# Kernel tuning notes

Measured on AMD Instinct MI355X. Metric: run time of the kernel, lower is better.

The kernel has to match this reference:

```python
import jax, jax.numpy as jnp
import numpy as np

B, N, M, D0, D, H, KW = 2, 512, 512, 1024, 100, 50, 7
K_SLOPE, X0_SIG = 20.0, 0.5  # LogisticActivation(x0=0.5, k=20), k not trained


def setup_inputs() -> dict:
    key = jax.random.key(0)
    ks = jax.random.split(key, 8)
    s = lambda k, shp: jax.random.normal(k, shp, jnp.float32) * 0.05
    return {
        "x0": jax.random.normal(ks[0], (B, N, D0), jnp.float32),
        "x1": jax.random.normal(ks[1], (B, M, D0), jnp.float32),
        "W_proj": s(ks[2], (D0, D)),
        "b_proj": jnp.zeros((D,), jnp.float32),
        "W_hid": s(ks[3], (2 * D, H)),
        "b_hid": jnp.zeros((H,), jnp.float32),
        "conv_w": s(ks[4], (1, H, KW, KW)),  # OIHW
        "conv_b": jnp.zeros((1,), jnp.float32),
        "theta": jnp.array([0.5], jnp.float32),
        "lambda_": jnp.array([0.3], jnp.float32),
        "gamma": jnp.array([0.2], jnp.float32),
    }


def reference(x0, x1, W_proj, b_proj, W_hid, b_hid, conv_w, conv_b, theta, lambda_, gamma):
    # --- embedding: FullyConnectedEmbed (Linear + ReLU) ---
    e0 = jax.nn.relu(x0 @ W_proj + b_proj)  # [B,N,D]
    e1 = jax.nn.relu(x1 @ W_proj + b_proj)  # [B,M,D]
    # --- contact: broadcast features -> 1x1 conv -> 7x7 conv -> sigmoid ---
    diff = jnp.abs(e0[:, :, None, :] - e1[:, None, :, :])   # [B,N,M,D]
    mul = e0[:, :, None, :] * e1[:, None, :, :]             # [B,N,M,D]
    Z = jnp.concatenate([diff, mul], axis=-1)               # [B,N,M,2D]
    Hh = jax.nn.relu(jnp.einsum('bnmc,ch->bhnm', Z, W_hid) + b_hid[None, :, None, None])
    C = jax.lax.conv_general_dilated(Hh, conv_w, (1, 1), 'SAME')
    C = jax.nn.sigmoid(C + conv_b[None, :, None, None])     # [B,1,N,M]
    # --- weighting matrix W (do_w=True) ---
    i = jnp.arange(N, dtype=jnp.float32)
    j = jnp.arange(M, dtype=jnp.float32)
    a = -jnp.square((i + 1 - (N + 1) / 2) / (-(N + 1) / 2))
    b = -jnp.square((j + 1 - (M + 1) / 2) / (-(M + 1) / 2))
    a = jnp.exp(lambda_ * a)                                 # [N]
    b = jnp.exp(lambda_ * b)                                 # [M]
    W = (1 - theta[0]) * (a[:, None] * b[None, :]) + theta[0]
    yhat = C * W                                             # [B,1,N,M]
    # --- global pooling: mean/var threshold + ratio ---
    mu = jnp.mean(yhat, axis=(1, 2, 3), keepdims=True)
    sigma = jnp.var(yhat, axis=(1, 2, 3), ddof=1, keepdims=True)  # torch.var is unbiased
    Q = jax.nn.relu(yhat - mu - gamma[0] * sigma)
    phat = jnp.sum(Q, axis=(1, 2, 3)) / (jnp.sum(jnp.sign(Q), axis=(1, 2, 3)) + 1)
    # --- LogisticActivation ---
    return jnp.clip(1.0 / (1.0 + jnp.exp(-K_SLOPE * (phat - X0_SIG))), 0.0, 1.0)  # [B]
```

## Files before the change

### kernel.cpp

```cpp
#include <hip/hip_runtime.h>
#include <hip/hip_bf16.h>

static constexpr int Bc   = 2;
static constexpr int Nc   = 512;
static constexpr int Mc   = 512;
static constexpr int D0c  = 1024;
static constexpr int Dc   = 100;
static constexpr int Hc   = 50;
static constexpr long long NMc = (long long)Nc * Mc;

typedef __attribute__((ext_vector_type(8))) short short8v;
typedef __attribute__((ext_vector_type(4))) float f32x4;

__device__ __forceinline__ unsigned pk_hi(float a, float b) {
  return __builtin_amdgcn_perm(__float_as_uint(b), __float_as_uint(a), 0x07060302u);
}
__device__ __forceinline__ float trunc16(float x) {
  return __uint_as_float(__float_as_uint(x) & 0xffff0000u);
}

__global__ __launch_bounds__(512) void k_embed(
    const float* __restrict__ x0, const float* __restrict__ x1,
    const float* __restrict__ Wp, const float* __restrict__ bp,
    float* __restrict__ e0, float* __restrict__ e1)
{
  __shared__ float xs[8][1024];
  const int t   = threadIdx.x;
  const int rg0 = blockIdx.x * 8;

  #pragma unroll
  for (int i = 0; i < 4; ++i) {
    const int idx = i*512 + t;
    const int r   = idx >> 8;
    const int c4  = idx & 255;
    const int rgs = rg0 + r;
    const float* src = (rgs < Bc*Nc) ? (x0 + (size_t)rgs * D0c)
                                     : (x1 + (size_t)(rgs - Bc*Nc) * D0c);
    *(float4*)&xs[r][c4*4] = *(const float4*)&src[c4*4];
  }
  __syncthreads();

  const int c = t & 127;
  const int q = t >> 7;
  if (c < Dc) {
    const int row0 = q*2, row1 = q*2 + 1;
    float acc0 = 0.f, acc1 = 0.f;
    for (int k = 0; k < D0c; k += 8) {
      float w[8];
      #pragma unroll
      for (int u = 0; u < 8; ++u) w[u] = Wp[(k+u)*Dc + c];
      const float4 xa0 = *(const float4*)&xs[row0][k];
      const float4 xb0 = *(const float4*)&xs[row0][k+4];
      const float4 xa1 = *(const float4*)&xs[row1][k];
      const float4 xb1 = *(const float4*)&xs[row1][k+4];
      acc0 = fmaf(xa0.x, w[0], acc0); acc1 = fmaf(xa1.x, w[0], acc1);
      acc0 = fmaf(xa0.y, w[1], acc0); acc1 = fmaf(xa1.y, w[1], acc1);
      acc0 = fmaf(xa0.z, w[2], acc0); acc1 = fmaf(xa1.z, w[2], acc1);
      acc0 = fmaf(xa0.w, w[3], acc0); acc1 = fmaf(xa1.w, w[3], acc1);
      acc0 = fmaf(xb0.x, w[4], acc0); acc1 = fmaf(xb1.x, w[4], acc1);
      acc0 = fmaf(xb0.y, w[5], acc0); acc1 = fmaf(xb1.y, w[5], acc1);
      acc0 = fmaf(xb0.z, w[6], acc0); acc1 = fmaf(xb1.z, w[6], acc1);
      acc0 = fmaf(xb0.w, w[7], acc0); acc1 = fmaf(xb1.w, w[7], acc1);
    }
    const float bias = bp[c];
    {
      const int rg = rg0 + row0;
      const float v = fmaxf(acc0 + bias, 0.f);
      if (rg < Bc*Nc) e0[(size_t)rg*Dc + c] = v;
      else            e1[(size_t)(rg - Bc*Nc)*Dc + c] = v;
    }
    {
      const int rg = rg0 + row1;
      const float v = fmaxf(acc1 + bias, 0.f);
      if (rg < Bc*Nc) e0[(size_t)rg*Dc + c] = v;
      else            e1[(size_t)(rg - Bc*Nc)*Dc + c] = v;
    }
  }
}

__global__ __launch_bounds__(64) void k_wsplit(
    const float* __restrict__ Whid, uint4* __restrict__ wsplit)
{
  const int fi = blockIdx.x;
  const int s  = fi >> 3;
  const int ht = (fi >> 1) & 3;
  const int hl = fi & 1;
  const int lane = threadIdx.x;
  const int h_loc = lane & 15, g = lane >> 4;
  const int h = ht*16 + h_loc;
  uint dw[4] = {0u,0u,0u,0u};
  #pragma unroll
  for (int j = 0; j < 8; ++j) {
    const int p = j >> 2, q = j & 3;
    const int d = s*16 + g*4 + q;
    float wv = (h < Hc && d < Dc) ? Whid[(size_t)(p*Dc + d)*Hc + h] : 0.f;
    const uint bits = __float_as_uint(wv);
    const uint hi_bits = bits & 0xffff0000u;
    uint e16;
    if (hl == 0) e16 = hi_bits >> 16;
    else {
      const float lo = wv - __uint_as_float(hi_bits);
      e16 = __float_as_uint(lo) >> 16;
    }
    dw[j >> 1] |= e16 << (16 * (j & 1));
  }
  uint4 v; v.x = dw[0]; v.y = dw[1]; v.z = dw[2]; v.w = dw[3];
  wsplit[fi*64 + lane] = v;
}

__global__ __launch_bounds__(256, 4) void k_hh(
    const float* __restrict__ e0, const float* __restrict__ e1,
    const uint4* __restrict__ wsplit, const float* __restrict__ bhid,
    float* __restrict__ hh, int slab_n0, int slabh)
{
  const int b   = blockIdx.z;
  const int lr0 = blockIdx.y * 2;
  const int n0base = slab_n0 + lr0;
  if (n0base + 1 < 0 || n0base >= Nc) return;

  __shared__ float e1T[32][116];
  __shared__ float e0s[2][112];
  __shared__ float biasl[64];
  __shared__ float ldsT[4][16][17];

  const int t   = threadIdx.x;
  const int m0b = blockIdx.x * 32;

  {
    const int row = t >> 3;
    const int cb  = (t & 7) * 4;
    const float* src = e1 + (size_t)(b*Mc + m0b + row) * Dc;
    #pragma unroll
    for (int pass = 0; pass < 4; ++pass) {
      const int col = cb + pass*32;
      if (col < 112) {
        float4 v = {0.f,0.f,0.f,0.f};
        if (col < Dc) v = *(const float4*)&src[col];
        *(float4*)&e1T[row][col] = v;
      }
    }
  }
  {
    const int nl2 = t >> 7, col = t & 127;
    if (col < 112) {
      const int n = n0base + nl2;
      float v = 0.f;
      if ((unsigned)n < (unsigned)Nc && col < Dc)
        v = e0[(size_t)(b*Nc + n)*Dc + col];
      e0s[nl2][col] = v;
    }
  }
  if (t < 64) biasl[t] = (t < Hc) ? bhid[t] : 0.f;
  __syncthreads();

  const int w = t >> 6, lane = t & 63;
  const int cl = lane & 15, g = lane >> 4;
  const int nl   = w >> 1;
  const int mrow = (w & 1) * 16 + cl;

  f32x4 acc0 = {0.f,0.f,0.f,0.f}, acc1 = {0.f,0.f,0.f,0.f};
  f32x4 acc2 = {0.f,0.f,0.f,0.f}, acc3 = {0.f,0.f,0.f,0.f};

  union U { uint4 u; short8v v; };
  const uint4* __restrict__ wq = wsplit + lane;

  #pragma unroll
  for (int s = 0; s < 7; ++s) {
    const int d0 = s*16 + g*4;
    const float4 E1 = *(const float4*)&e1T[mrow][d0];
    const float4 E0 = *(const float4*)&e0s[nl][d0];

    const float df0 = fabsf(E0.x - E1.x), df1 = fabsf(E0.y - E1.y),
                df2 = fabsf(E0.z - E1.z), df3 = fabsf(E0.w - E1.w);
    const float pm0 = E0.x*E1.x, pm1 = E0.y*E1.y,
                pm2 = E0.z*E1.z, pm3 = E0.w*E1.w;

    U ahi, alo;
    ahi.u.x = pk_hi(df0, df1); ahi.u.y = pk_hi(df2, df3);
    ahi.u.z = pk_hi(pm0, pm1); ahi.u.w = pk_hi(pm2, pm3);
    alo.u.x = pk_hi(df0 - trunc16(df0), df1 - trunc16(df1));
    alo.u.y = pk_hi(df2 - trunc16(df2), df3 - trunc16(df3));
    alo.u.z = pk_hi(pm0 - trunc16(pm0), pm1 - trunc16(pm1));
    alo.u.w = pk_hi(pm2 - trunc16(pm2), pm3 - trunc16(pm3));

    #pragma unroll
    for (int ht = 0; ht < 4; ++ht) {
      U whi, wlo;
      whi.u = wq[((s*4 + ht)*2 + 0)*64];
      wlo.u = wq[((s*4 + ht)*2 + 1)*64];
      f32x4* ac = (ht == 0) ? &acc0 : (ht == 1) ? &acc1 : (ht == 2) ? &acc2 : &acc3;
      *ac = __builtin_amdgcn_mfma_f32_16x16x32_bf16(ahi.v, whi.v, *ac, 0, 0, 0);
      *ac = __builtin_amdgcn_mfma_f32_16x16x32_bf16(alo.v, whi.v, *ac, 0, 0, 0);
      *ac = __builtin_amdgcn_mfma_f32_16x16x32_bf16(ahi.v, wlo.v, *ac, 0, 0, 0);
    }
  }

  const int n = n0base + nl;
  const bool nvalid = (unsigned)n < (unsigned)Nc;
  const int S = slabh * Mc;
  float* hhp = hh + ((size_t)b*Hc)*S + (size_t)(lr0 + nl)*Mc
                  + (m0b + (w & 1)*16 + cl) + (size_t)g*S;

  const f32x4 accs[4] = {acc0, acc1, acc2, acc3};
  #pragma unroll
  for (int ht = 0; ht < 4; ++ht) {
    #pragma unroll
    for (int r = 0; r < 4; ++r) ldsT[w][cl][g*4 + r] = accs[ht][r];
    #pragma unroll
    for (int p = 0; p < 4; ++p) {
      const int hl2 = p*4 + g;
      const int h = ht*16 + hl2;
      if (h < Hc && nvalid) {
        const float v = fmaxf(ldsT[w][hl2][cl] + biasl[h], 0.f);
        hhp[(size_t)((ht*16 + p*4) * S)] = v;
      }
    }
  }
}

__global__ __launch_bounds__(256) void k_conv(
    const float* __restrict__ hh, const float* __restrict__ cw,
    const float* __restrict__ cb, const float* __restrict__ theta,
    const float* __restrict__ lam, float* __restrict__ yhat,
    double* __restrict__ gacc, int n_begin, int slabh)
{
  __shared__ float tile[2][38*40];
  __shared__ double red[2][4];
  const int t  = threadIdx.x;
  const int b  = blockIdx.z;
  const int n0 = n_begin + blockIdx.y * 32;
  const int m0 = blockIdx.x * 32;

  const int rr = t >> 3;
  const int c0 = 4 * (t & 7);

  float stg[6];
  auto issue = [&](int h) {
    #pragma unroll
    for (int it = 0; it < 6; ++it) {
      const int idx = it*256 + t;
      float v = 0.f;
      if (idx < 38*38) {
        const int r = idx / 38, c = idx - r*38;
        const int gn = n0 - 3 + r, gm = m0 - 3 + c;
        if ((unsigned)gn < (unsigned)Nc && (unsigned)gm < (unsigned)Mc)
          v = hh[(((size_t)(b*Hc + h))*slabh + (gn - n_begin + 3))*Mc + gm];
      }
      stg[it] = v;
    }
  };
  auto commit = [&](int buf) {
    #pragma unroll
    for (int it = 0; it < 6; ++it) {
      const int idx = it*256 + t;
      if (idx < 38*38) {
        const int r = idx / 38, c = idx - r*38;
        tile[buf][r*40 + c] = stg[it];
      }
    }
  };

  issue(0); commit(0);
  __syncthreads();

  float acc0 = 0.f, acc1 = 0.f, acc2 = 0.f, acc3 = 0.f;
  for (int h = 0; h < Hc; ++h) {
    if (h + 1 < Hc) issue(h + 1);
    const int buf = h & 1;
    const float* __restrict__ cp = cw + h*49;
    #pragma unroll
    for (int dn = 0; dn < 7; ++dn) {
      const float* tp = &tile[buf][(rr+dn)*40 + c0];
      const float4 wa = *(const float4*)tp;
      const float4 wb = *(const float4*)(tp+4);
      const float2 wc = *(const float2*)(tp+8);
      const float w_[10] = {wa.x,wa.y,wa.z,wa.w, wb.x,wb.y,wb.z,wb.w, wc.x,wc.y};
      #pragma unroll
      for (int dm = 0; dm < 7; ++dm) {
        const float wv = cp[dn*7 + dm];
        acc0 = fmaf(w_[dm],   wv, acc0);
        acc1 = fmaf(w_[dm+1], wv, acc1);
        acc2 = fmaf(w_[dm+2], wv, acc2);
        acc3 = fmaf(w_[dm+3], wv, acc3);
      }
    }
    if (h + 1 < Hc) { commit((h+1) & 1); __syncthreads(); }
  }

  const float th  = theta[0];
  const float lm  = lam[0];
  const float cbv = cb[0];
  const int n = n0 + rr;
  const int m = m0 + c0;
  const float half1 = 0.5f * (float)(Nc + 1);
  const float inv   = 1.0f / half1;
  const float ti  = ((float)(n+1) - half1) * inv;
  const float av  = expf(-lm * ti * ti);
  float y[4];
  double s = 0.0, ss = 0.0;
  const float a_[4] = {acc0, acc1, acc2, acc3};
  #pragma unroll
  for (int j = 0; j < 4; ++j) {
    const float tj = ((float)(m+1+j) - half1) * inv;
    const float bv = expf(-lm * tj * tj);
    const float sg = 1.f / (1.f + expf(-(a_[j] + cbv)));
    y[j] = sg * ((1.f - th) * av * bv + th);
    s  += (double)y[j];
    ss += (double)y[j] * (double)y[j];
  }
  float4 yv; yv.x = y[0]; yv.y = y[1]; yv.z = y[2]; yv.w = y[3];
  *(float4*)&yhat[((size_t)(b*Nc + n))*Mc + m] = yv;

  for (int off = 32; off > 0; off >>= 1) {
    s  += __shfl_down(s,  off);
    ss += __shfl_down(ss, off);
  }
  const int wave = t >> 6, lane = t & 63;
  if (lane == 0) { red[0][wave] = s; red[1][wave] = ss; }
  __syncthreads();
  if (t == 0) {
    atomicAdd(&gacc[b*4 + 0], red[0][0] + red[0][1] + red[0][2] + red[0][3]);
    atomicAdd(&gacc[b*4 + 1], red[1][0] + red[1][1] + red[1][2] + red[1][3]);
  }
}

__global__ __launch_bounds__(256) void k_q(
    const float* __restrict__ yhat, double* __restrict__ gacc,
    const float* __restrict__ gamma)
{
  const int tid = blockIdx.x * 256 + threadIdx.x;
  const int b = blockIdx.x >> 8;
  const float4 y = ((const float4*)yhat)[tid];
  const double sum = gacc[b*4 + 0], ssq = gacc[b*4 + 1];
  const double mu  = sum / (double)NMc;
  const double var = (ssq - sum * mu) / ((double)NMc - 1.0);
  const double thr = mu + (double)gamma[0] * var;

  double sq = 0.0; int c = 0;
  double q;
  q = (double)y.x - thr; if (q > 0.0) { sq += q; ++c; }
  q = (double)y.y - thr; if (q > 0.0) { sq += q; ++c; }
  q = (double)y.z - thr; if (q > 0.0) { sq += q; ++c; }
  q = (double)y.w - thr; if (q > 0.0) { sq += q; ++c; }

  for (int off = 32; off > 0; off >>= 1) {
    sq += __shfl_down(sq, off);
    c  += __shfl_down(c,  off);
  }
  __shared__ double sr[4];
  __shared__ int    cr[4];
  const int wave = threadIdx.x >> 6, lane = threadIdx.x & 63;
  if (lane == 0) { sr[wave] = sq; cr[wave] = c; }
  __syncthreads();
  if (threadIdx.x == 0) {
    atomicAdd(&gacc[b*4 + 2], sr[0] + sr[1] + sr[2] + sr[3]);
    atomicAdd(&gacc[b*4 + 3], (double)(cr[0] + cr[1] + cr[2] + cr[3]));
  }
}

__global__ void k_out(const double* __restrict__ gacc, float* __restrict__ out)
{
  const int t = threadIdx.x;
  if (t < Bc) {
    const double phat = gacc[t*4 + 2] / (gacc[t*4 + 3] + 1.0);
    double v = 1.0 / (1.0 + exp(-20.0 * (phat - 0.5)));
    v = fmin(fmax(v, 0.0), 1.0);
    out[t] = (float)v;
  }
}

extern "C" void kernel_launch(void* const* d_in, const int* in_sizes, int n_in,
                              void* d_out, int out_size, void* d_ws, size_t ws_size,
                              hipStream_t stream)
{
  const float* x0 = (const float*)d_in[0];
  const float* x1 = (const float*)d_in[1];
  const float* Wp = (const float*)d_in[2];
  const float* bp = (const float*)d_in[3];
  const float* Wh = (const float*)d_in[4];
  const float* bh = (const float*)d_in[5];
  const float* cw = (const float*)d_in[6];
  const float* cb = (const float*)d_in[7];
  const float* th = (const float*)d_in[8];
  const float* lm = (const float*)d_in[9];
  const float* gm = (const float*)d_in[10];
  float* out = (float*)d_out;
  (void)in_sizes; (void)n_in; (void)out_size;

  int slabrows, nslab;
  if      (ws_size >= (size_t)109232128) { slabrows = 512; nslab = 1; }
  else if (ws_size >= (size_t)56803328)  { slabrows = 256; nslab = 2; }
  else                                    { slabrows = 128; nslab = 4; }
  const int slabh = slabrows + 6;
  const size_t hh_bytes = (size_t)slabh * 204800;

  char* ws = (char*)d_ws;
  float*  e0   = (float*)(ws);
  float*  e1   = (float*)(ws + 409600);
  double* gacc = (double*)(ws + 819200);
  uint4*  wsp  = (uint4*)(ws + 884736);
  float*  hh   = (float*)(ws + 1048576);
  float*  yhat = (float*)(ws + 1048576 + hh_bytes);

  hipMemsetAsync(gacc, 0, 64, stream);
  k_wsplit<<<dim3(56), dim3(64), 0, stream>>>(Wh, wsp);
  k_embed<<<dim3(256), dim3(512), 0, stream>>>(x0, x1, Wp, bp, e0, e1);
  for (int s = 0; s < nslab; ++s) {
    const int n_begin = s * slabrows;
    k_hh  <<<dim3(16, slabh/2, 2), dim3(256), 0, stream>>>(
        e0, e1, wsp, bh, hh, n_begin - 3, slabh);
    k_conv<<<dim3(16, slabrows / 32, 2), dim3(256), 0, stream>>>(
        hh, cw, cb, th, lm, yhat, gacc, n_begin, slabh);
  }
  k_q  <<<dim3(512), dim3(256), 0, stream>>>(yhat, gacc, gm);
  k_out<<<dim3(1),   dim3(64),  0, stream>>>(gacc, out);
}
```

Baseline: 283.7 us.

## Store hidden maps as bf16, split conv over channel halves, fuse small kernels

Result: slower. 382.0 us (+34.6%).

```diff
diff --git a/kernel.cpp b/kernel.cpp
--- a/kernel.cpp
+++ b/kernel.cpp
@@ -18,14 +18,52 @@
 __device__ __forceinline__ float trunc16(float x) {
   return __uint_as_float(__float_as_uint(x) & 0xffff0000u);
 }
-
-__global__ __launch_bounds__(512) void k_embed(
+__device__ __forceinline__ unsigned short f2bf_rne(float x) {
+  const unsigned b = __float_as_uint(x);
+  const unsigned r = b + 0x7fffu + ((b >> 16) & 1u);
+  return (unsigned short)(r >> 16);
+}
+
+__global__ __launch_bounds__(512) void k_prep(
     const float* __restrict__ x0, const float* __restrict__ x1,
     const float* __restrict__ Wp, const float* __restrict__ bp,
-    float* __restrict__ e0, float* __restrict__ e1)
-{
+    const float* __restrict__ Whid,
+    float* __restrict__ e0, float* __restrict__ e1,
+    uint4* __restrict__ wsplit, double* __restrict__ gacc)
+{
+  const int t = threadIdx.x;
+  if (blockIdx.x == 256) {
+    if (t < 18) ((int*)gacc)[t] = 0;
+    const int grp = t >> 6, lane = t & 63;
+    const int h_loc = lane & 15, g = lane >> 4;
+    for (int fi = grp; fi < 56; fi += 8) {
+      const int s  = fi >> 3;
+      const int ht = (fi >> 1) & 3;
+      const int hl = fi & 1;
+      const int h = ht*16 + h_loc;
+      uint dw[4] = {0u,0u,0u,0u};
+      #pragma unroll
+      for (int j = 0; j < 8; ++j) {
+        const int p = j >> 2, q = j & 3;
+        const int d = s*16 + g*4 + q;
+        float wv = (h < Hc && d < Dc) ? Whid[(size_t)(p*Dc + d)*Hc + h] : 0.f;
+        const uint bits = __float_as_uint(wv);
+        const uint hi_bits = bits & 0xffff0000u;
+        uint e16;
+        if (hl == 0) e16 = hi_bits >> 16;
+        else {
+          const float lo = wv - __uint_as_float(hi_bits);
+          e16 = __float_as_uint(lo) >> 16;
+        }
+        dw[j >> 1] |= e16 << (16 * (j & 1));
+      }
+      uint4 v; v.x = dw[0]; v.y = dw[1]; v.z = dw[2]; v.w = dw[3];
+      wsplit[fi*64 + lane] = v;
+    }
+    return;
+  }
+
   __shared__ float xs[8][1024];
-  const int t   = threadIdx.x;
   const int rg0 = blockIdx.x * 8;
 
   #pragma unroll
@@ -78,40 +116,10 @@
   }
 }
 
-__global__ __launch_bounds__(64) void k_wsplit(
-    const float* __restrict__ Whid, uint4* __restrict__ wsplit)
-{
-  const int fi = blockIdx.x;
-  const int s  = fi >> 3;
-  const int ht = (fi >> 1) & 3;
-  const int hl = fi & 1;
-  const int lane = threadIdx.x;
-  const int h_loc = lane & 15, g = lane >> 4;
-  const int h = ht*16 + h_loc;
-  uint dw[4] = {0u,0u,0u,0u};
-  #pragma unroll
-  for (int j = 0; j < 8; ++j) {
-    const int p = j >> 2, q = j & 3;
-    const int d = s*16 + g*4 + q;
-    float wv = (h < Hc && d < Dc) ? Whid[(size_t)(p*Dc + d)*Hc + h] : 0.f;
-    const uint bits = __float_as_uint(wv);
-    const uint hi_bits = bits & 0xffff0000u;
-    uint e16;
-    if (hl == 0) e16 = hi_bits >> 16;
-    else {
-      const float lo = wv - __uint_as_float(hi_bits);
-      e16 = __float_as_uint(lo) >> 16;
-    }
-    dw[j >> 1] |= e16 << (16 * (j & 1));
-  }
-  uint4 v; v.x = dw[0]; v.y = dw[1]; v.z = dw[2]; v.w = dw[3];
-  wsplit[fi*64 + lane] = v;
-}
-
 __global__ __launch_bounds__(256, 4) void k_hh(
     const float* __restrict__ e0, const float* __restrict__ e1,
     const uint4* __restrict__ wsplit, const float* __restrict__ bhid,
-    float* __restrict__ hh, int slab_n0, int slabh)
+    unsigned short* __restrict__ hh, int slab_n0, int slabh)
 {
   const int b   = blockIdx.z;
   const int lr0 = blockIdx.y * 2;
@@ -198,7 +206,7 @@
   const int n = n0base + nl;
   const bool nvalid = (unsigned)n < (unsigned)Nc;
   const int S = slabh * Mc;
-  float* hhp = hh + ((size_t)b*Hc)*S + (size_t)(lr0 + nl)*Mc
+  unsigned short* hhp = hh + ((size_t)b*Hc)*S + (size_t)(lr0 + nl)*Mc
                   + (m0b + (w & 1)*16 + cl) + (size_t)g*S;
 
   const f32x4 accs[4] = {acc0, acc1, acc2, acc3};
@@ -212,22 +220,21 @@
       const int h = ht*16 + hl2;
       if (h < Hc && nvalid) {
         const float v = fmaxf(ldsT[w][hl2][cl] + biasl[h], 0.f);
-        hhp[(size_t)((ht*16 + p*4) * S)] = v;
+        hhp[(size_t)((ht*16 + p*4) * S)] = f2bf_rne(v);
       }
     }
   }
 }
 
 __global__ __launch_bounds__(256) void k_conv(
-    const float* __restrict__ hh, const float* __restrict__ cw,
-    const float* __restrict__ cb, const float* __restrict__ theta,
-    const float* __restrict__ lam, float* __restrict__ yhat,
-    double* __restrict__ gacc, int n_begin, int slabh)
+    const unsigned short* __restrict__ hh, const float* __restrict__ cw,
+    float* __restrict__ part0, float* __restrict__ part1,
+    int n_begin, int slabh)
 {
   __shared__ float tile[2][38*40];
-  __shared__ double red[2][4];
   const int t  = threadIdx.x;
-  const int b  = blockIdx.z;
+  const int b  = blockIdx.z >> 1;
+  const int g  = blockIdx.z & 1;
   const int n0 = n_begin + blockIdx.y * 32;
   const int m0 = blockIdx.x * 32;
 
@@ -244,7 +251,8 @@
         const int r = idx / 38, c = idx - r*38;
         const int gn = n0 - 3 + r, gm = m0 - 3 + c;
         if ((unsigned)gn < (unsigned)Nc && (unsigned)gm < (unsigned)Mc)
-          v = hh[(((size_t)(b*Hc + h))*slabh + (gn - n_begin + 3))*Mc + gm];
+          v = __uint_as_float(
+              (unsigned)hh[(((size_t)(b*Hc + h))*slabh + (gn - n_begin + 3))*Mc + gm] << 16);
       }
       stg[it] = v;
     }
@@ -260,14 +268,15 @@
     }
   };
 
-  issue(0); commit(0);
+  const int h0 = g * 25;
+  issue(h0); commit(0);
   __syncthreads();
 
   float acc0 = 0.f, acc1 = 0.f, acc2 = 0.f, acc3 = 0.f;
-  for (int h = 0; h < Hc; ++h) {
-    if (h + 1 < Hc) issue(h + 1);
-    const int buf = h & 1;
-    const float* __restrict__ cp = cw + h*49;
+  for (int hi = 0; hi < 25; ++hi) {
+    if (hi + 1 < 25) issue(h0 + hi + 1);
+    const int buf = hi & 1;
+    const float* __restrict__ cp = cw + (h0 + hi)*49;
     #pragma unroll
     for (int dn = 0; dn < 7; ++dn) {
       const float* tp = &tile[buf][(rr+dn)*40 + c0];
@@ -284,23 +293,40 @@
         acc3 = fmaf(w_[dm+3], wv, acc3);
       }
     }
-    if (h + 1 < Hc) { commit((h+1) & 1); __syncthreads(); }
-  }
-
-  const float th  = theta[0];
-  const float lm  = lam[0];
-  const float cbv = cb[0];
+    if (hi + 1 < 25) { commit((hi+1) & 1); __syncthreads(); }
+  }
+
+  float* __restrict__ dst = g ? part1 : part0;
   const int n = n0 + rr;
-  const int m = m0 + c0;
+  float4 v; v.x = acc0; v.y = acc1; v.z = acc2; v.w = acc3;
+  *(float4*)&dst[((size_t)b*Nc + n)*Mc + (m0 + c0)] = v;
+}
+
+__global__ __launch_bounds__(256) void k_post(
+    const float* __restrict__ part0, const float* __restrict__ part1,
+    const float* __restrict__ cb, const float* __restrict__ theta,
+    const float* __restrict__ lam, float* __restrict__ yhat,
+    double* __restrict__ gacc)
+{
+  __shared__ double red[2][4];
+  const int t = threadIdx.x;
+  const int px0 = (blockIdx.x*256 + t)*2;
+  const int b = px0 >> 18;
+  const int p = px0 & 262143;
+  const int n = p >> 9, m = p & 511;
+
+  const float2 pa = *(const float2*)&part0[px0];
+  const float2 pb = *(const float2*)&part1[px0];
+  const float cbv = cb[0], th = theta[0], lm = lam[0];
   const float half1 = 0.5f * (float)(Nc + 1);
   const float inv   = 1.0f / half1;
-  const float ti  = ((float)(n+1) - half1) * inv;
-  const float av  = expf(-lm * ti * ti);
-  float y[4];
-  double s = 0.0, ss = 0.0;
-  const float a_[4] = {acc0, acc1, acc2, acc3};
+  const float ti = ((float)(n+1) - half1) * inv;
+  const float av = expf(-lm * ti * ti);
+
+  const float a_[2] = {pa.x + pb.x, pa.y + pb.y};
+  float y[2]; double s = 0.0, ss = 0.0;
   #pragma unroll
-  for (int j = 0; j < 4; ++j) {
+  for (int j = 0; j < 2; ++j) {
     const float tj = ((float)(m+1+j) - half1) * inv;
     const float bv = expf(-lm * tj * tj);
     const float sg = 1.f / (1.f + expf(-(a_[j] + cbv)));
@@ -308,8 +334,8 @@
     s  += (double)y[j];
     ss += (double)y[j] * (double)y[j];
   }
-  float4 yv; yv.x = y[0]; yv.y = y[1]; yv.z = y[2]; yv.w = y[3];
-  *(float4*)&yhat[((size_t)(b*Nc + n))*Mc + m] = yv;
+  float2 yv; yv.x = y[0]; yv.y = y[1];
+  *(float2*)&yhat[px0] = yv;
 
   for (int off = 32; off > 0; off >>= 1) {
     s  += __shfl_down(s,  off);
@@ -326,7 +352,8 @@
 
 __global__ __launch_bounds__(256) void k_q(
     const float* __restrict__ yhat, double* __restrict__ gacc,
-    const float* __restrict__ gamma)
+    const float* __restrict__ gamma, float* __restrict__ out,
+    int* __restrict__ counter)
 {
   const int tid = blockIdx.x * 256 + threadIdx.x;
   const int b = blockIdx.x >> 8;
@@ -355,17 +382,18 @@
   if (threadIdx.x == 0) {
     atomicAdd(&gacc[b*4 + 2], sr[0] + sr[1] + sr[2] + sr[3]);
     atomicAdd(&gacc[b*4 + 3], (double)(cr[0] + cr[1] + cr[2] + cr[3]));
-  }
-}
-
-__global__ void k_out(const double* __restrict__ gacc, float* __restrict__ out)
-{
-  const int t = threadIdx.x;
-  if (t < Bc) {
-    const double phat = gacc[t*4 + 2] / (gacc[t*4 + 3] + 1.0);
-    double v = 1.0 / (1.0 + exp(-20.0 * (phat - 0.5)));
-    v = fmin(fmax(v, 0.0), 1.0);
-    out[t] = (float)v;
+    __threadfence();
+    const int ticket = atomicAdd(counter, 1);
+    if (ticket == 511) {
+      __threadfence();
+      #pragma unroll
+      for (int bb = 0; bb < Bc; ++bb) {
+        const double phat = gacc[bb*4 + 2] / (gacc[bb*4 + 3] + 1.0);
+        double v = 1.0 / (1.0 + exp(-20.0 * (phat - 0.5)));
+        v = fmin(fmax(v, 0.0), 1.0);
+        out[bb] = (float)v;
+      }
+    }
   }
 }
 
@@ -388,30 +416,31 @@
   (void)in_sizes; (void)n_in; (void)out_size;
 
   int slabrows, nslab;
-  if      (ws_size >= (size_t)109232128) { slabrows = 512; nslab = 1; }
-  else if (ws_size >= (size_t)56803328)  { slabrows = 256; nslab = 2; }
-  else                                    { slabrows = 128; nslab = 4; }
+  if      (ws_size >= (size_t)62000000) { slabrows = 512; nslab = 1; }
+  else if (ws_size >= (size_t)35000000) { slabrows = 256; nslab = 2; }
+  else                                   { slabrows = 128; nslab = 4; }
   const int slabh = slabrows + 6;
-  const size_t hh_bytes = (size_t)slabh * 204800;
+  const size_t hh_bytes = (size_t)slabh * 102400;
 
   char* ws = (char*)d_ws;
   float*  e0   = (float*)(ws);
   float*  e1   = (float*)(ws + 409600);
   double* gacc = (double*)(ws + 819200);
+  int*    cnt  = (int*)(ws + 819200 + 64);
   uint4*  wsp  = (uint4*)(ws + 884736);
-  float*  hh   = (float*)(ws + 1048576);
-  float*  yhat = (float*)(ws + 1048576 + hh_bytes);
-
-  hipMemsetAsync(gacc, 0, 64, stream);
-  k_wsplit<<<dim3(56), dim3(64), 0, stream>>>(Wh, wsp);
-  k_embed<<<dim3(256), dim3(512), 0, stream>>>(x0, x1, Wp, bp, e0, e1);
+  unsigned short* hh = (unsigned short*)(ws + 1048576);
+  float*  part0 = (float*)(ws + 1048576 + hh_bytes);
+  float*  part1 = part0 + (size_t)Bc*Nc*Mc;
+  float*  yhat  = part1 + (size_t)Bc*Nc*Mc;
+
+  k_prep<<<dim3(257), dim3(512), 0, stream>>>(x0, x1, Wp, bp, Wh, e0, e1, wsp, gacc);
   for (int s = 0; s < nslab; ++s) {
     const int n_begin = s * slabrows;
     k_hh  <<<dim3(16, slabh/2, 2), dim3(256), 0, stream>>>(
         e0, e1, wsp, bh, hh, n_begin - 3, slabh);
-    k_conv<<<dim3(16, slabrows / 32, 2), dim3(256), 0, stream>>>(
-        hh, cw, cb, th, lm, yhat, gacc, n_begin, slabh);
-  }
-  k_q  <<<dim3(512), dim3(256), 0, stream>>>(yhat, gacc, gm);
-  k_out<<<dim3(1),   dim3(64),  0, stream>>>(gacc, out);
-}
+    k_conv<<<dim3(16, slabrows / 32, 4), dim3(256), 0, stream>>>(
+        hh, cw, part0, part1, n_begin, slabh);
+  }
+  k_post<<<dim3(1024), dim3(256), 0, stream>>>(part0, part1, cb, th, lm, yhat, gacc);
+  k_q   <<<dim3(512),  dim3(256), 0, stream>>>(yhat, gacc, gm, out, cnt);
+}
```
